# Kernel optimization log

Hardware: AMD Instinct MI355X
Metric: run time of the kernel (lower is better)

## Reference

```python
import jax, jax.numpy as jnp
import numpy as np

N, E, IN, H, C = 50000, 800000, 128, 4, 32


def setup_inputs() -> dict:
    key = jax.random.key(0)
    ks = jax.random.split(key, 10)
    scale = 1.0 / np.sqrt(IN)
    x = jax.random.normal(ks[0], (N, IN), dtype=jnp.float32)
    edge_index = jax.random.randint(ks[1], (2, E), 0, N, dtype=jnp.int64)
    Wq = jax.random.uniform(ks[2], (IN, H * C), jnp.float32, -scale, scale)
    bq = jnp.zeros((H * C,), jnp.float32)
    Wk = jax.random.uniform(ks[3], (IN, H * C), jnp.float32, -scale, scale)
    bk = jnp.zeros((H * C,), jnp.float32)
    Wv = jax.random.uniform(ks[4], (IN, H * C), jnp.float32, -scale, scale)
    bv = jnp.zeros((H * C,), jnp.float32)
    Wskip = jax.random.uniform(ks[5], (IN, H * C), jnp.float32, -scale, scale)
    bskip = jnp.zeros((H * C,), jnp.float32)
    return {"x": x, "edge_index": edge_index, "Wq": Wq, "bq": bq,
            "Wk": Wk, "bk": bk, "Wv": Wv, "bv": bv,
            "Wskip": Wskip, "bskip": bskip}


def reference(x, edge_index, Wq, bq, Wk, bk, Wv, bv, Wskip, bskip):
    # PyG TransformerConv: edge messages flow src -> dst
    src, dst = edge_index[0], edge_index[1]
    q = (x @ Wq + bq).reshape(N, H, C)
    k = (x @ Wk + bk).reshape(N, H, C)
    v = (x @ Wv + bv).reshape(N, H, C)
    # per-edge attention logits [E, H]
    alpha = jnp.einsum('ehc,ehc->eh', q[dst], k[src]) / jnp.sqrt(jnp.float32(C))
    # scatter-softmax over incoming edges of each dst node
    m = jax.ops.segment_max(alpha, dst, num_segments=N)  # [N, H]
    ex = jnp.exp(alpha - m[dst])
    denom = jax.ops.segment_sum(ex, dst, num_segments=N)  # [N, H]
    w = ex / denom[dst]  # [E, H]
    # weighted scatter-add of values
    agg = jax.ops.segment_sum(v[src] * w[:, :, None], dst, num_segments=N)  # [N,H,C]
    out = agg.reshape(N, H * C) + x @ Wskip + bskip
    return out
```

## Files before the change

### kernel.cpp

```cpp
#include <hip/hip_runtime.h>
#include <hip/hip_bf16.h>

#define NNODES 50000
#define NEDGES 800000
#define FDIM   128
#define NHEADS 4
#define NSCANB ((NNODES + 1023) / 1024)
#define NBLK   782
#define NT16   (NBLK * 4)
#define NFULL  3125

typedef __attribute__((ext_vector_type(8))) short  bf16x8;
typedef __attribute__((ext_vector_type(4))) float  f32x4;

static __device__ __forceinline__ unsigned short f2bf(float f) {
    __hip_bfloat16 h = __float2bfloat16(f);
    return *reinterpret_cast<unsigned short*>(&h);
}
static __device__ __forceinline__ float bf2f(unsigned short u) {
    return __uint_as_float(((unsigned int)u) << 16);
}

__global__ __launch_bounds__(256) void tgd_cvt_xa(const float* __restrict__ x,
                                                  unsigned short* __restrict__ xa)
{
    __shared__ unsigned short lds[16 * 136];
    const int gt  = blockIdx.x;
    const int tid = threadIdx.x;

    if (gt < NFULL) {
        const float* src = x + (size_t)gt * 2048 + tid * 8;
        float4 f0 = *reinterpret_cast<const float4*>(src);
        float4 f1 = *reinterpret_cast<const float4*>(src + 4);
        const int row = tid >> 4;
        const int col = (tid & 15) * 8;
        unsigned short* d = &lds[row * 136 + col];
        d[0]=f2bf(f0.x); d[1]=f2bf(f0.y); d[2]=f2bf(f0.z); d[3]=f2bf(f0.w);
        d[4]=f2bf(f1.x); d[5]=f2bf(f1.y); d[6]=f2bf(f1.z); d[7]=f2bf(f1.w);
    }
    __syncthreads();

    const int lane = tid & 63;
    const int ks   = tid >> 6;
    const int row  = lane & 15;
    const int k0   = ks * 32 + (lane >> 4) * 8;
    unsigned short u[8];
    if (gt < NFULL) {
        #pragma unroll
        for (int j = 0; j < 8; ++j) u[j] = lds[row * 136 + k0 + j];
    } else {
        #pragma unroll
        for (int j = 0; j < 8; ++j) u[j] = 0;
    }
    *reinterpret_cast<uint4*>(&xa[((size_t)gt * 256 + tid) * 8]) =
        *reinterpret_cast<uint4*>(u);
}

__global__ __launch_bounds__(256) void tgd_cvt_w(
    const float* __restrict__ Wq, const float* __restrict__ Wk,
    const float* __restrict__ Wv, const float* __restrict__ Wsk,
    unsigned short* __restrict__ Wt2)
{
    int t = blockIdx.x * 256 + threadIdx.x;
    if (t >= 4 * 8 * 4 * 64) return;
    int m    = t >> 11;
    int ct   = (t >> 8) & 7;
    int ks   = (t >> 6) & 3;
    int lane = t & 63;
    int c  = ct * 16 + (lane & 15);
    int k0 = ks * 32 + (lane >> 4) * 8;
    const float* W = (m == 0) ? Wq : (m == 1) ? Wk : (m == 2) ? Wv : Wsk;
    unsigned short u[8];
    #pragma unroll
    for (int j = 0; j < 8; ++j)
        u[j] = f2bf(W[(size_t)(k0 + j) * FDIM + c]);
    *reinterpret_cast<uint4*>(&Wt2[(size_t)t * 8]) = *reinterpret_cast<uint4*>(u);
}

__global__ __launch_bounds__(512) void tgd_gemm_mfma(
    const unsigned short* __restrict__ xa, const unsigned short* __restrict__ Wt2,
    const float* __restrict__ bq, const float* __restrict__ bk,
    const float* __restrict__ bv, const float* __restrict__ bsk,
    unsigned short* __restrict__ qb, unsigned short* __restrict__ kv,
    float* __restrict__ outp)
{
    __shared__ float st[64 * 128];
    unsigned short* sth = (unsigned short*)st;

    const int tid  = threadIdx.x;
    const int wave = tid >> 6, lane = tid & 63;
    const int mp   = wave >> 2;
    const int wr   = wave & 3;
    const int l16  = lane & 15, lhi = lane >> 4;
    const int gt   = blockIdx.x * 4 + wr;
    const int base = blockIdx.x * 64;

    bf16x8 a[4];
    #pragma unroll
    for (int ks = 0; ks < 4; ++ks)
        a[ks] = *reinterpret_cast<const bf16x8*>(
            xa + ((size_t)(gt * 4 + ks) * 64 + lane) * 8);

    f32x4 acc[2][8];
    #pragma unroll
    for (int m2 = 0; m2 < 2; ++m2)
        #pragma unroll
        for (int ct = 0; ct < 8; ++ct)
            acc[m2][ct] = (f32x4){0.f, 0.f, 0.f, 0.f};

    #pragma unroll
    for (int ks = 0; ks < 4; ++ks) {
        #pragma unroll
        for (int m2 = 0; m2 < 2; ++m2) {
            const int m = mp * 2 + m2;
            const unsigned short* wb =
                Wt2 + ((size_t)((m * 8 * 4 + ks) * 64) + lane) * 8;
            #pragma unroll
            for (int ct = 0; ct < 8; ++ct) {
                bf16x8 b = *reinterpret_cast<const bf16x8*>(wb + (size_t)ct * 2048);
                acc[m2][ct] = __builtin_amdgcn_mfma_f32_16x16x32_bf16(
                    a[ks], b, acc[m2][ct], 0, 0, 0);
            }
        }
    }

    const int rowl0 = wr * 16 + lhi * 4;

    if (mp == 0) {
        #pragma unroll
        for (int ct = 0; ct < 8; ++ct) {
            int col = ct * 16 + l16;
            float bval = bq[col];
            #pragma unroll
            for (int r = 0; r < 4; ++r)
                sth[(rowl0 + r) * 128 + col] = f2bf(acc[0][ct][r] + bval);
        }
    }
    __syncthreads();
    #pragma unroll
    for (int i = 0; i < 2; ++i) {
        int idx = i * 512 + tid;
        int row = idx >> 4, c8 = idx & 15;
        if (base + row < NNODES)
            *reinterpret_cast<uint4*>(&qb[(size_t)(base + row) * 128 + c8 * 8]) =
                *reinterpret_cast<const uint4*>(&sth[row * 128 + c8 * 8]);
    }
    __syncthreads();

    if (mp == 1) {
        #pragma unroll
        for (int ct = 0; ct < 8; ++ct) {
            int col = ct * 16 + l16;
            float bval = bsk[col];
            #pragma unroll
            for (int r = 0; r < 4; ++r)
                st[(rowl0 + r) * 128 + col] = acc[1][ct][r] + bval;
        }
    }
    __syncthreads();
    #pragma unroll
    for (int i = 0; i < 4; ++i) {
        int idx = i * 512 + tid;
        int row = idx >> 5, c4 = idx & 31;
        if (base + row < NNODES)
            *reinterpret_cast<float4*>(&outp[(size_t)(base + row) * FDIM + c4 * 4]) =
                *reinterpret_cast<const float4*>(&st[row * 128 + c4 * 4]);
    }
    __syncthreads();

    {
        const int off  = (mp == 0) ? 0 : 128;
        const int m2s  = (mp == 0) ? 1 : 0;
        const float* bias = (mp == 0) ? bk : bv;
        #pragma unroll
        for (int ct = 0; ct < 8; ++ct) {
            int col = ct * 16 + l16;
            float bval = bias[col];
            #pragma unroll
            for (int r = 0; r < 4; ++r)
                sth[(rowl0 + r) * 256 + off + col] = f2bf(acc[m2s][ct][r] + bval);
        }
    }
    __syncthreads();
    #pragma unroll
    for (int i = 0; i < 4; ++i) {
        int idx = i * 512 + tid;
        int row = idx >> 5, c8 = idx & 31;
        if (base + row < NNODES)
            *reinterpret_cast<uint4*>(&kv[(size_t)(base + row) * 256 + c8 * 8]) =
                *reinterpret_cast<const uint4*>(&sth[row * 256 + c8 * 8]);
    }
}

__global__ __launch_bounds__(256) void tgd_hist(const int* __restrict__ ei,
                                                int* __restrict__ deg)
{
    int t = blockIdx.x * 256 + threadIdx.x;
    if (t < NEDGES) atomicAdd(&deg[ei[NEDGES + t]], 1);
}

__global__ __launch_bounds__(1024) void tgd_scan1(const int* __restrict__ deg,
                                                  int* __restrict__ rowptr,
                                                  int* __restrict__ bsum)
{
    __shared__ int buf[1024];
    const int tid = threadIdx.x;
    const int i   = blockIdx.x * 1024 + tid;
    int d = (i < NNODES) ? deg[i] : 0;
    buf[tid] = d;
    __syncthreads();
    #pragma unroll
    for (int off = 1; off < 1024; off <<= 1) {
        int t2 = (tid >= off) ? buf[tid - off] : 0;
        __syncthreads();
        buf[tid] += t2;
        __syncthreads();
    }
    if (i < NNODES) rowptr[i + 1] = buf[tid];
    if (tid == 1023) bsum[blockIdx.x] = buf[1023];
}

__global__ __launch_bounds__(64) void tgd_scan2(const int* __restrict__ bsum,
                                                int* __restrict__ boff)
{
    int lane = threadIdx.x;
    int v = (lane < NSCANB) ? bsum[lane] : 0;
    int own = v;
    #pragma unroll
    for (int off = 1; off < 64; off <<= 1) {
        int t = __shfl_up(v, off);
        if (lane >= off) v += t;
    }
    if (lane < NSCANB) boff[lane] = v - own;
}

__global__ __launch_bounds__(1024) void tgd_scan3(const int* __restrict__ deg,
                                                  const int* __restrict__ boff,
                                                  int* __restrict__ rowptr,
                                                  int* __restrict__ ofs)
{
    const int i = blockIdx.x * 1024 + threadIdx.x;
    if (i < NNODES) {
        int r = rowptr[i + 1] + boff[blockIdx.x];
        rowptr[i + 1] = r;
        ofs[i] = r - deg[i];
    }
    if (i == 0) rowptr[0] = 0;
}

__global__ __launch_bounds__(256) void tgd_build(const int* __restrict__ ei,
                                                 int* __restrict__ ofs,
                                                 int* __restrict__ csr)
{
    int t = blockIdx.x * 256 + threadIdx.x;
    if (t >= NEDGES) return;
    int src = ei[t];
    int dst = ei[NEDGES + t];
    int pos = atomicAdd(&ofs[dst], 1);
    csr[pos] = src;
}

__global__ __launch_bounds__(256) void tgd_agg(
    const int* __restrict__ csr, const int* __restrict__ rowptr,
    const unsigned short* __restrict__ qb, const unsigned short* __restrict__ kv,
    float* __restrict__ outp)
{
    const int node = blockIdx.x * 4 + (threadIdx.x >> 6);
    const int lane = threadIdx.x & 63;
    if (node >= NNODES) return;
    const int start = rowptr[node];
    const int end   = rowptr[node + 1];
    if (start == end) return;

    const bool isK = (lane < 32);
    float4 qv = {0.f, 0.f, 0.f, 0.f};
    if (isK) {
        ushort4 qu = *reinterpret_cast<const ushort4*>(&qb[(size_t)node * FDIM + lane * 4]);
        qv.x = bf2f(qu.x); qv.y = bf2f(qu.y); qv.z = bf2f(qu.z); qv.w = bf2f(qu.w);
    }
    const float inv = 0.17677669529663687f;

    float  den = 0.0f;
    float4 acc = {0.f, 0.f, 0.f, 0.f};

    for (int base = start; base < end; base += 64) {
        const int cnt = min(64, end - base);
        int myid = (lane < cnt) ? csr[base + lane] : 0;

        int j = 0;
        for (; j + 3 < cnt; j += 4) {
            int s0 = __shfl(myid, j);
            int s1 = __shfl(myid, j + 1);
            int s2 = __shfl(myid, j + 2);
            int s3 = __shfl(myid, j + 3);
            ushort4 r0 = *reinterpret_cast<const ushort4*>(&kv[(size_t)s0 * 256 + lane * 4]);
            ushort4 r1 = *reinterpret_cast<const ushort4*>(&kv[(size_t)s1 * 256 + lane * 4]);
            ushort4 r2 = *reinterpret_cast<const ushort4*>(&kv[(size_t)s2 * 256 + lane * 4]);
            ushort4 r3 = *reinterpret_cast<const ushort4*>(&kv[(size_t)s3 * 256 + lane * 4]);

            float a0 = bf2f(r0.x), a1 = bf2f(r0.y), a2 = bf2f(r0.z), a3 = bf2f(r0.w);
            float b0 = bf2f(r1.x), b1 = bf2f(r1.y), b2 = bf2f(r1.z), b3 = bf2f(r1.w);
            float c0 = bf2f(r2.x), c1 = bf2f(r2.y), c2 = bf2f(r2.z), c3 = bf2f(r2.w);
            float d0 = bf2f(r3.x), d1 = bf2f(r3.y), d2 = bf2f(r3.z), d3 = bf2f(r3.w);

            float sA = qv.x*a0 + qv.y*a1 + qv.z*a2 + qv.w*a3;
            float sB = qv.x*b0 + qv.y*b1 + qv.z*b2 + qv.w*b3;
            float sC = qv.x*c0 + qv.y*c1 + qv.z*c2 + qv.w*c3;
            float sD = qv.x*d0 + qv.y*d1 + qv.z*d2 + qv.w*d3;
            sA += __shfl_xor(sA, 1);  sB += __shfl_xor(sB, 1);
            sC += __shfl_xor(sC, 1);  sD += __shfl_xor(sD, 1);
            sA += __shfl_xor(sA, 2);  sB += __shfl_xor(sB, 2);
            sC += __shfl_xor(sC, 2);  sD += __shfl_xor(sD, 2);
            sA += __shfl_xor(sA, 4);  sB += __shfl_xor(sB, 4);
            sC += __shfl_xor(sC, 4);  sD += __shfl_xor(sD, 4);
            float wA = __expf(sA * inv);
            float wB = __expf(sB * inv);
            float wC = __expf(sC * inv);
            float wD = __expf(sD * inv);
            wA = __shfl_xor(wA, 32);
            wB = __shfl_xor(wB, 32);
            wC = __shfl_xor(wC, 32);
            wD = __shfl_xor(wD, 32);
            if (!isK) {
                den += (wA + wB) + (wC + wD);
                acc.x += wA*a0 + wB*b0 + wC*c0 + wD*d0;
                acc.y += wA*a1 + wB*b1 + wC*c1 + wD*d1;
                acc.z += wA*a2 + wB*b2 + wC*c2 + wD*d2;
                acc.w += wA*a3 + wB*b3 + wC*c3 + wD*d3;
            }
        }
        for (; j + 1 < cnt; j += 2) {
            int s0 = __shfl(myid, j);
            int s1 = __shfl(myid, j + 1);
            ushort4 r0 = *reinterpret_cast<const ushort4*>(&kv[(size_t)s0 * 256 + lane * 4]);
            ushort4 r1 = *reinterpret_cast<const ushort4*>(&kv[(size_t)s1 * 256 + lane * 4]);
            float a0 = bf2f(r0.x), a1 = bf2f(r0.y), a2 = bf2f(r0.z), a3 = bf2f(r0.w);
            float b0 = bf2f(r1.x), b1 = bf2f(r1.y), b2 = bf2f(r1.z), b3 = bf2f(r1.w);
            float sA = qv.x*a0 + qv.y*a1 + qv.z*a2 + qv.w*a3;
            float sB = qv.x*b0 + qv.y*b1 + qv.z*b2 + qv.w*b3;
            sA += __shfl_xor(sA, 1);  sB += __shfl_xor(sB, 1);
            sA += __shfl_xor(sA, 2);  sB += __shfl_xor(sB, 2);
            sA += __shfl_xor(sA, 4);  sB += __shfl_xor(sB, 4);
            float wA = __expf(sA * inv);
            float wB = __expf(sB * inv);
            wA = __shfl_xor(wA, 32);
            wB = __shfl_xor(wB, 32);
            if (!isK) {
                den += wA + wB;
                acc.x += wA*a0 + wB*b0;
                acc.y += wA*a1 + wB*b1;
                acc.z += wA*a2 + wB*b2;
                acc.w += wA*a3 + wB*b3;
            }
        }
        if (j < cnt) {
            int s0 = __shfl(myid, j);
            ushort4 r0 = *reinterpret_cast<const ushort4*>(&kv[(size_t)s0 * 256 + lane * 4]);
            float a0 = bf2f(r0.x), a1 = bf2f(r0.y), a2 = bf2f(r0.z), a3 = bf2f(r0.w);
            float sA = qv.x*a0 + qv.y*a1 + qv.z*a2 + qv.w*a3;
            sA += __shfl_xor(sA, 1);
            sA += __shfl_xor(sA, 2);
            sA += __shfl_xor(sA, 4);
            float wA = __expf(sA * inv);
            wA = __shfl_xor(wA, 32);
            if (!isK) {
                den += wA;
                acc.x += wA*a0; acc.y += wA*a1; acc.z += wA*a2; acc.w += wA*a3;
            }
        }
    }

    if (!isK) {
        float invd = 1.0f / den;
        float4* o = reinterpret_cast<float4*>(&outp[(size_t)node * FDIM + (lane - 32) * 4]);
        float4 cur = *o;
        cur.x += acc.x * invd;
        cur.y += acc.y * invd;
        cur.z += acc.z * invd;
        cur.w += acc.w * invd;
        *o = cur;
    }
}

extern "C" void kernel_launch(void* const* d_in, const int* in_sizes, int n_in,
                              void* d_out, int out_size, void* d_ws, size_t ws_size,
                              hipStream_t stream) {
    const float* x   = (const float*)d_in[0];
    const int*   ei  = (const int*)  d_in[1];
    const float* Wq  = (const float*)d_in[2];
    const float* bq  = (const float*)d_in[3];
    const float* Wk  = (const float*)d_in[4];
    const float* bk  = (const float*)d_in[5];
    const float* Wv  = (const float*)d_in[6];
    const float* bv  = (const float*)d_in[7];
    const float* Wsk = (const float*)d_in[8];
    const float* bsk = (const float*)d_in[9];
    float* outp = (float*)d_out;

    unsigned short* qb  = (unsigned short*)d_ws;
    unsigned short* kv  = qb + (size_t)NNODES * FDIM;
    unsigned short* xa  = kv + (size_t)NNODES * 256;
    unsigned short* Wt2 = xa + (size_t)NT16 * 2048;
    int* deg    = (int*)(Wt2 + 4 * FDIM * FDIM);
    int* rowptr = deg + NNODES;
    int* ofs    = rowptr + NNODES + 1;
    int* csr    = ofs + NNODES;
    int* bsum   = csr + NEDGES;
    int* boff   = bsum + NSCANB;

    hipMemsetAsync(deg, 0, (size_t)NNODES * sizeof(int), stream);

    tgd_cvt_xa<<<NT16, 256, 0, stream>>>(x, xa);
    tgd_cvt_w<<<(4 * 8 * 4 * 64 + 255) / 256, 256, 0, stream>>>(Wq, Wk, Wv, Wsk, Wt2);

    tgd_gemm_mfma<<<NBLK, 512, 0, stream>>>(
        xa, Wt2, bq, bk, bv, bsk, qb, kv, outp);

    tgd_hist<<<(NEDGES + 255) / 256, 256, 0, stream>>>(ei, deg);
    tgd_scan1<<<NSCANB, 1024, 0, stream>>>(deg, rowptr, bsum);
    tgd_scan2<<<1, 64, 0, stream>>>(bsum, boff);
    tgd_scan3<<<NSCANB, 1024, 0, stream>>>(deg, boff, rowptr, ofs);
    tgd_build<<<(NEDGES + 255) / 256, 256, 0, stream>>>(ei, ofs, csr);
    tgd_agg<<<(NNODES + 3) / 4, 256, 0, stream>>>(csr, rowptr, qb, kv, outp);
}
```

Baseline: 296.3 us.

## Fuse prep/hist/scan launches and switch q/k/v storage to fp16 with dot2

Merges the weight conversion with zeroing the degree array, folds the degree histogram into the x-conversion kernel, and removes the single-block scan2 by having each scan3 block reduce the preceding block sums itself. This cuts kernel launches and a memset. Separately, q, k and v are now stored as fp16 instead of bf16, so the aggregation can use packed fdot2 for the attention logits, and the 2-edge tail loop is simplified to a 1-edge loop. fp16 has a narrower range than bf16, which could overflow on unusual inputs.

```diff
diff --git a/kernel.cpp b/kernel.cpp
--- a/kernel.cpp
+++ b/kernel.cpp
@@ -1,5 +1,6 @@
 #include <hip/hip_runtime.h>
 #include <hip/hip_bf16.h>
+#include <hip/hip_fp16.h>
 
 #define NNODES 50000
 #define NEDGES 800000
@@ -12,17 +13,61 @@
 
 typedef __attribute__((ext_vector_type(8))) short  bf16x8;
 typedef __attribute__((ext_vector_type(4))) float  f32x4;
+typedef _Float16 h2f __attribute__((ext_vector_type(2)));
 
 static __device__ __forceinline__ unsigned short f2bf(float f) {
     __hip_bfloat16 h = __float2bfloat16(f);
     return *reinterpret_cast<unsigned short*>(&h);
 }
-static __device__ __forceinline__ float bf2f(unsigned short u) {
-    return __uint_as_float(((unsigned int)u) << 16);
+static __device__ __forceinline__ unsigned short f2h(float f) {
+    __half h = __float2half(f);
+    return *reinterpret_cast<unsigned short*>(&h);
+}
+static __device__ __forceinline__ h2f u2h2(unsigned int u) {
+    return *reinterpret_cast<h2f*>(&u);
+}
+static __device__ __forceinline__ float hdot4(h2f a01, h2f a23, h2f b01, h2f b23) {
+#if __has_builtin(__builtin_amdgcn_fdot2)
+    return __builtin_amdgcn_fdot2(a01, b01,
+           __builtin_amdgcn_fdot2(a23, b23, 0.0f, false), false);
+#else
+    return (float)a01[0]*(float)b01[0] + (float)a01[1]*(float)b01[1]
+         + (float)a23[0]*(float)b23[0] + (float)a23[1]*(float)b23[1];
+#endif
+}
+
+__global__ __launch_bounds__(256) void tgd_prep(
+    const float* __restrict__ Wq, const float* __restrict__ Wk,
+    const float* __restrict__ Wv, const float* __restrict__ Wsk,
+    unsigned short* __restrict__ Wt2, int* __restrict__ deg)
+{
+    const int b = blockIdx.x;
+    if (b < 32) {
+        int t = b * 256 + threadIdx.x;
+        int m    = t >> 11;
+        int ct   = (t >> 8) & 7;
+        int ks   = (t >> 6) & 3;
+        int lane = t & 63;
+        int c  = ct * 16 + (lane & 15);
+        int k0 = ks * 32 + (lane >> 4) * 8;
+        const float* W = (m == 0) ? Wq : (m == 1) ? Wk : (m == 2) ? Wv : Wsk;
+        unsigned short u[8];
+        #pragma unroll
+        for (int j = 0; j < 8; ++j)
+            u[j] = f2bf(W[(size_t)(k0 + j) * FDIM + c]);
+        *reinterpret_cast<uint4*>(&Wt2[(size_t)t * 8]) = *reinterpret_cast<uint4*>(u);
+    } else {
+        int i0 = ((b - 32) * 256 + threadIdx.x) * 4;
+        #pragma unroll
+        for (int j = 0; j < 4; ++j)
+            if (i0 + j < NNODES) deg[i0 + j] = 0;
+    }
 }
 
 __global__ __launch_bounds__(256) void tgd_cvt_xa(const float* __restrict__ x,
-                                                  unsigned short* __restrict__ xa)
+                                                  unsigned short* __restrict__ xa,
+                                                  const int* __restrict__ ei,
+                                                  int* __restrict__ deg)
 {
     __shared__ unsigned short lds[16 * 136];
     const int gt  = blockIdx.x;
@@ -54,27 +99,9 @@
     }
     *reinterpret_cast<uint4*>(&xa[((size_t)gt * 256 + tid) * 8]) =
         *reinterpret_cast<uint4*>(u);
-}
-
-__global__ __launch_bounds__(256) void tgd_cvt_w(
-    const float* __restrict__ Wq, const float* __restrict__ Wk,
-    const float* __restrict__ Wv, const float* __restrict__ Wsk,
-    unsigned short* __restrict__ Wt2)
-{
-    int t = blockIdx.x * 256 + threadIdx.x;
-    if (t >= 4 * 8 * 4 * 64) return;
-    int m    = t >> 11;
-    int ct   = (t >> 8) & 7;
-    int ks   = (t >> 6) & 3;
-    int lane = t & 63;
-    int c  = ct * 16 + (lane & 15);
-    int k0 = ks * 32 + (lane >> 4) * 8;
-    const float* W = (m == 0) ? Wq : (m == 1) ? Wk : (m == 2) ? Wv : Wsk;
-    unsigned short u[8];
-    #pragma unroll
-    for (int j = 0; j < 8; ++j)
-        u[j] = f2bf(W[(size_t)(k0 + j) * FDIM + c]);
-    *reinterpret_cast<uint4*>(&Wt2[(size_t)t * 8]) = *reinterpret_cast<uint4*>(u);
+
+    int e = gt * 256 + tid;
+    if (e < NEDGES) atomicAdd(&deg[ei[NEDGES + e]], 1);
 }
 
 __global__ __launch_bounds__(512) void tgd_gemm_mfma(
@@ -133,7 +160,7 @@
             float bval = bq[col];
             #pragma unroll
             for (int r = 0; r < 4; ++r)
-                sth[(rowl0 + r) * 128 + col] = f2bf(acc[0][ct][r] + bval);
+                sth[(rowl0 + r) * 128 + col] = f2h(acc[0][ct][r] + bval);
         }
     }
     __syncthreads();
@@ -178,7 +205,7 @@
             float bval = bias[col];
             #pragma unroll
             for (int r = 0; r < 4; ++r)
-                sth[(rowl0 + r) * 256 + off + col] = f2bf(acc[m2s][ct][r] + bval);
+                sth[(rowl0 + r) * 256 + off + col] = f2h(acc[m2s][ct][r] + bval);
         }
     }
     __syncthreads();
@@ -192,13 +219,6 @@
     }
 }
 
-__global__ __launch_bounds__(256) void tgd_hist(const int* __restrict__ ei,
-                                                int* __restrict__ deg)
-{
-    int t = blockIdx.x * 256 + threadIdx.x;
-    if (t < NEDGES) atomicAdd(&deg[ei[NEDGES + t]], 1);
-}
-
 __global__ __launch_bounds__(1024) void tgd_scan1(const int* __restrict__ deg,
                                                   int* __restrict__ rowptr,
                                                   int* __restrict__ bsum)
@@ -220,28 +240,23 @@
     if (tid == 1023) bsum[blockIdx.x] = buf[1023];
 }
 
-__global__ __launch_bounds__(64) void tgd_scan2(const int* __restrict__ bsum,
-                                                int* __restrict__ boff)
-{
-    int lane = threadIdx.x;
-    int v = (lane < NSCANB) ? bsum[lane] : 0;
-    int own = v;
-    #pragma unroll
-    for (int off = 1; off < 64; off <<= 1) {
-        int t = __shfl_up(v, off);
-        if (lane >= off) v += t;
-    }
-    if (lane < NSCANB) boff[lane] = v - own;
-}
-
 __global__ __launch_bounds__(1024) void tgd_scan3(const int* __restrict__ deg,
-                                                  const int* __restrict__ boff,
+                                                  const int* __restrict__ bsum,
                                                   int* __restrict__ rowptr,
                                                   int* __restrict__ ofs)
 {
-    const int i = blockIdx.x * 1024 + threadIdx.x;
+    __shared__ int sboff;
+    const int tid = threadIdx.x;
+    if (tid < 64) {
+        int v = (tid < blockIdx.x) ? bsum[tid] : 0;
+        #pragma unroll
+        for (int m = 32; m >= 1; m >>= 1) v += __shfl_xor(v, m);
+        if (tid == 0) sboff = v;
+    }
+    __syncthreads();
+    const int i = blockIdx.x * 1024 + tid;
     if (i < NNODES) {
-        int r = rowptr[i + 1] + boff[blockIdx.x];
+        int r = rowptr[i + 1] + sboff;
         rowptr[i + 1] = r;
         ofs[i] = r - deg[i];
     }
@@ -273,10 +288,10 @@
     if (start == end) return;
 
     const bool isK = (lane < 32);
-    float4 qv = {0.f, 0.f, 0.f, 0.f};
+    h2f q01 = (h2f)(_Float16)0, q23 = (h2f)(_Float16)0;
     if (isK) {
-        ushort4 qu = *reinterpret_cast<const ushort4*>(&qb[(size_t)node * FDIM + lane * 4]);
-        qv.x = bf2f(qu.x); qv.y = bf2f(qu.y); qv.z = bf2f(qu.z); qv.w = bf2f(qu.w);
+        uint2 qu = *reinterpret_cast<const uint2*>(&qb[(size_t)node * FDIM + lane * 4]);
+        q01 = u2h2(qu.x); q23 = u2h2(qu.y);
     }
     const float inv = 0.17677669529663687f;
 
@@ -293,20 +308,20 @@
             int s1 = __shfl(myid, j + 1);
             int s2 = __shfl(myid, j + 2);
             int s3 = __shfl(myid, j + 3);
-            ushort4 r0 = *reinterpret_cast<const ushort4*>(&kv[(size_t)s0 * 256 + lane * 4]);
-            ushort4 r1 = *reinterpret_cast<const ushort4*>(&kv[(size_t)s1 * 256 + lane * 4]);
-            ushort4 r2 = *reinterpret_cast<const ushort4*>(&kv[(size_t)s2 * 256 + lane * 4]);
-            ushort4 r3 = *reinterpret_cast<const ushort4*>(&kv[(size_t)s3 * 256 + lane * 4]);
-
-            float a0 = bf2f(r0.x), a1 = bf2f(r0.y), a2 = bf2f(r0.z), a3 = bf2f(r0.w);
-            float b0 = bf2f(r1.x), b1 = bf2f(r1.y), b2 = bf2f(r1.z), b3 = bf2f(r1.w);
-            float c0 = bf2f(r2.x), c1 = bf2f(r2.y), c2 = bf2f(r2.z), c3 = bf2f(r2.w);
-            float d0 = bf2f(r3.x), d1 = bf2f(r3.y), d2 = bf2f(r3.z), d3 = bf2f(r3.w);
-
-            float sA = qv.x*a0 + qv.y*a1 + qv.z*a2 + qv.w*a3;
-            float sB = qv.x*b0 + qv.y*b1 + qv.z*b2 + qv.w*b3;
-            float sC = qv.x*c0 + qv.y*c1 + qv.z*c2 + qv.w*c3;
-            float sD = qv.x*d0 + qv.y*d1 + qv.z*d2 + qv.w*d3;
+            uint2 r0 = *reinterpret_cast<const uint2*>(&kv[(size_t)s0 * 256 + lane * 4]);
+            uint2 r1 = *reinterpret_cast<const uint2*>(&kv[(size_t)s1 * 256 + lane * 4]);
+            uint2 r2 = *reinterpret_cast<const uint2*>(&kv[(size_t)s2 * 256 + lane * 4]);
+            uint2 r3 = *reinterpret_cast<const uint2*>(&kv[(size_t)s3 * 256 + lane * 4]);
+
+            h2f a01 = u2h2(r0.x), a23 = u2h2(r0.y);
+            h2f b01 = u2h2(r1.x), b23 = u2h2(r1.y);
+            h2f c01 = u2h2(r2.x), c23 = u2h2(r2.y);
+            h2f d01 = u2h2(r3.x), d23 = u2h2(r3.y);
+
+            float sA = hdot4(q01, q23, a01, a23);
+            float sB = hdot4(q01, q23, b01, b23);
+            float sC = hdot4(q01, q23, c01, c23);
+            float sD = hdot4(q01, q23, d01, d23);
             sA += __shfl_xor(sA, 1);  sB += __shfl_xor(sB, 1);
             sC += __shfl_xor(sC, 1);  sD += __shfl_xor(sD, 1);
             sA += __shfl_xor(sA, 2);  sB += __shfl_xor(sB, 2);
@@ -323,41 +338,17 @@
             wD = __shfl_xor(wD, 32);
             if (!isK) {
                 den += (wA + wB) + (wC + wD);
-                acc.x += wA*a0 + wB*b0 + wC*c0 + wD*d0;
-                acc.y += wA*a1 + wB*b1 + wC*c1 + wD*d1;
-                acc.z += wA*a2 + wB*b2 + wC*c2 + wD*d2;
-                acc.w += wA*a3 + wB*b3 + wC*c3 + wD*d3;
+                acc.x += wA*(float)a01[0] + wB*(float)b01[0] + wC*(float)c01[0] + wD*(float)d01[0];
+                acc.y += wA*(float)a01[1] + wB*(float)b01[1] + wC*(float)c01[1] + wD*(float)d01[1];
+                acc.z += wA*(float)a23[0] + wB*(float)b23[0] + wC*(float)c23[0] + wD*(float)d23[0];
+                acc.w += wA*(float)a23[1] + wB*(float)b23[1] + wC*(float)c23[1] + wD*(float)d23[1];
             }
         }
-        for (; j + 1 < cnt; j += 2) {
+        for (; j < cnt; ++j) {
             int s0 = __shfl(myid, j);
-            int s1 = __shfl(myid, j + 1);
-            ushort4 r0 = *reinterpret_cast<const ushort4*>(&kv[(size_t)s0 * 256 + lane * 4]);
-            ushort4 r1 = *reinterpret_cast<const ushort4*>(&kv[(size_t)s1 * 256 + lane * 4]);
-            float a0 = bf2f(r0.x), a1 = bf2f(r0.y), a2 = bf2f(r0.z), a3 = bf2f(r0.w);
-            float b0 = bf2f(r1.x), b1 = bf2f(r1.y), b2 = bf2f(r1.z), b3 = bf2f(r1.w);
-            float sA = qv.x*a0 + qv.y*a1 + qv.z*a2 + qv.w*a3;
-            float sB = qv.x*b0 + qv.y*b1 + qv.z*b2 + qv.w*b3;
-            sA += __shfl_xor(sA, 1);  sB += __shfl_xor(sB, 1);
-            sA += __shfl_xor(sA, 2);  sB += __shfl_xor(sB, 2);
-            sA += __shfl_xor(sA, 4);  sB += __shfl_xor(sB, 4);
-            float wA = __expf(sA * inv);
-            float wB = __expf(sB * inv);
-            wA = __shfl_xor(wA, 32);
-            wB = __shfl_xor(wB, 32);
-            if (!isK) {
-                den += wA + wB;
-                acc.x += wA*a0 + wB*b0;
-                acc.y += wA*a1 + wB*b1;
-                acc.z += wA*a2 + wB*b2;
-                acc.w += wA*a3 + wB*b3;
-            }
-        }
-        if (j < cnt) {
-            int s0 = __shfl(myid, j);
-            ushort4 r0 = *reinterpret_cast<const ushort4*>(&kv[(size_t)s0 * 256 + lane * 4]);
-            float a0 = bf2f(r0.x), a1 = bf2f(r0.y), a2 = bf2f(r0.z), a3 = bf2f(r0.w);
-            float sA = qv.x*a0 + qv.y*a1 + qv.z*a2 + qv.w*a3;
+            uint2 r0 = *reinterpret_cast<const uint2*>(&kv[(size_t)s0 * 256 + lane * 4]);
+            h2f a01 = u2h2(r0.x), a23 = u2h2(r0.y);
+            float sA = hdot4(q01, q23, a01, a23);
             sA += __shfl_xor(sA, 1);
             sA += __shfl_xor(sA, 2);
             sA += __shfl_xor(sA, 4);
@@ -365,7 +356,8 @@
             wA = __shfl_xor(wA, 32);
             if (!isK) {
                 den += wA;
-                acc.x += wA*a0; acc.y += wA*a1; acc.z += wA*a2; acc.w += wA*a3;
+                acc.x += wA*(float)a01[0]; acc.y += wA*(float)a01[1];
+                acc.z += wA*(float)a23[0]; acc.w += wA*(float)a23[1];
             }
         }
     }
@@ -406,20 +398,17 @@
     int* ofs    = rowptr + NNODES + 1;
     int* csr    = ofs + NNODES;
     int* bsum   = csr + NEDGES;
-    int* boff   = bsum + NSCANB;
-
-    hipMemsetAsync(deg, 0, (size_t)NNODES * sizeof(int), stream);
-
-    tgd_cvt_xa<<<NT16, 256, 0, stream>>>(x, xa);
-    tgd_cvt_w<<<(4 * 8 * 4 * 64 + 255) / 256, 256, 0, stream>>>(Wq, Wk, Wv, Wsk, Wt2);
+
+    tgd_prep<<<32 + NSCANB, 256, 0, stream>>>(Wq, Wk, Wv, Wsk, Wt2, deg);
+
+    tgd_cvt_xa<<<NT16, 256, 0, stream>>>(x, xa, ei, deg);
 
     tgd_gemm_mfma<<<NBLK, 512, 0, stream>>>(
         xa, Wt2, bq, bk, bv, bsk, qb, kv, outp);
 
-    tgd_hist<<<(NEDGES + 255) / 256, 256, 0, stream>>>(ei, deg);
     tgd_scan1<<<NSCANB, 1024, 0, stream>>>(deg, rowptr, bsum);
-    tgd_scan2<<<1, 64, 0, stream>>>(bsum, boff);
-    tgd_scan3<<<NSCANB, 1024, 0, stream>>>(deg, boff, rowptr, ofs);
+    tgd_scan3<<<NSCANB, 1024, 0, stream>>>(deg, bsum, rowptr, ofs);
     tgd_build<<<(NEDGES + 255) / 256, 256, 0, stream>>>(ei, ofs, csr);
+
     tgd_agg<<<(NNODES + 3) / 4, 256, 0, stream>>>(csr, rowptr, qb, kv, outp);
 }
```

After: 289.0 us. 1.03x faster.
